# Kernel tuning notes

Hardware: AMD Instinct MI355X
Metric: run time of the kernel (lower is better)

## Reference

```python
import jax, jax.numpy as jnp
import numpy as np
import math

D_MODEL = 1024
NUM_HEADS = 16
HEAD_DIM = D_MODEL // NUM_HEADS
CLAMP = 1e9


def setup_inputs() -> dict:
    key = jax.random.key(0)
    k1, k2, k3, k4, k5 = jax.random.split(key, 5)
    B, S = 2, 2048
    x = jax.random.normal(k1, (B, S, D_MODEL), dtype=jnp.float32)
    # torch Linear params, stored as [in, out] (y = x @ W + b)
    s1 = 1.0 / math.sqrt(D_MODEL)
    W_qkv = jax.random.uniform(k2, (D_MODEL, 3 * D_MODEL), jnp.float32, -s1, s1)
    b_qkv = jax.random.uniform(k3, (3 * D_MODEL,), jnp.float32, -s1, s1)
    W_out = jax.random.uniform(k4, (D_MODEL, D_MODEL), jnp.float32, -s1, s1)
    b_out = jax.random.uniform(k5, (D_MODEL,), jnp.float32, -s1, s1)
    return {"x": x, "W_qkv": W_qkv, "b_qkv": b_qkv, "W_out": W_out, "b_out": b_out}


def reference(x, W_qkv, b_qkv, W_out, b_out):
    B, S, D = x.shape
    qkv = x @ W_qkv + b_qkv                       # [B, S, 3*D]
    qkv = qkv.reshape(B, S, NUM_HEADS, 3 * HEAD_DIM).transpose(0, 2, 1, 3)  # [B, H, S, 3*hd]
    q, k, v = jnp.split(qkv, 3, axis=-1)          # each [B, H, S, hd]
    scale = 1.0 / math.sqrt(HEAD_DIM)
    scores = jnp.einsum('bhqd,bhkd->bhqk', q, k) * scale  # [B, H, S, S]
    causal = jnp.tril(jnp.ones((S, S), dtype=bool))
    scores = jnp.where(causal, scores, -jnp.inf)
    scores = jnp.clip(scores, -CLAMP, CLAMP)      # -inf -> -1e9, matching torch clamp
    attn = jax.nn.softmax(scores, axis=-1)
    values = jnp.einsum('bhqk,bhkd->bhqd', attn, v)        # [B, H, S, hd]
    values = values.transpose(0, 2, 1, 3).reshape(B, S, D)  # [B, S, D]
    out = values @ W_out + b_out
    # dropout is identity in eval mode
    return out
```

## Files before the change

### kernel.cpp

```cpp
#include <hip/hip_runtime.h>
#include <hip/hip_bf16.h>

#define D_MODEL 1024
#define NUM_HEADS 16
#define HEAD_DIM 64
#define SEQ 2048
#define BATCH 2
#define ROWS (BATCH * SEQ)

typedef unsigned short u16;
typedef __bf16 bf16x8 __attribute__((ext_vector_type(8)));
typedef float f32x4 __attribute__((ext_vector_type(4)));

__device__ inline u16 f2bfu(float f) {
  unsigned u = __float_as_uint(f);
  unsigned r = (u + 0x7fffu + ((u >> 16) & 1u)) >> 16;
  return (u16)r;
}

__device__ inline unsigned cvt_pk_bf16(float a, float b) {
#if __has_builtin(__builtin_amdgcn_cvt_pk_bf16_f32)
  auto r = __builtin_amdgcn_cvt_pk_bf16_f32(a, b);
  unsigned u;
  __builtin_memcpy(&u, &r, 4);
  return u;
#else
  return (unsigned)f2bfu(a) | ((unsigned)f2bfu(b) << 16);
#endif
}

__device__ inline f32x4 mfma16(bf16x8 a, bf16x8 b, f32x4 c) {
  return __builtin_amdgcn_mfma_f32_16x16x32_bf16(a, b, c, 0, 0, 0);
}

__device__ inline bf16x8 load_frag(const u16* p) {
  union { uint4 v; bf16x8 f; } u;
  u.v = *(const uint4*)p;
  return u.f;
}

__device__ inline void gload_lds16(const u16* g, u16* l) {
  __builtin_amdgcn_global_load_lds((const __attribute__((address_space(1))) void*)g,
                                   (__attribute__((address_space(3))) void*)l, 16, 0, 0);
}


__global__ __launch_bounds__(256) void prep_kernel(const float* __restrict__ x,
                                                   u16* __restrict__ xb,
                                                   const float* __restrict__ Wq,
                                                   u16* __restrict__ WqT,
                                                   const float* __restrict__ Wo,
                                                   u16* __restrict__ WoT) {
  __shared__ float t[32][33];
  const int bid = blockIdx.x;
  if (bid < 4096) {
    int i = bid * 256 + threadIdx.x;
    float4 v = ((const float4*)x)[i];
    uint2 o;
    o.x = cvt_pk_bf16(v.x, v.y);
    o.y = cvt_pk_bf16(v.z, v.w);
    ((uint2*)xb)[i] = o;
    return;
  }
  const float* W;
  u16* Wt;
  int N, tIdx;
  if (bid < 4096 + 3072) { W = Wq; Wt = WqT; N = 3072; tIdx = bid - 4096; }
  else                   { W = Wo; Wt = WoT; N = 1024; tIdx = bid - 7168; }
  const int k0 = (tIdx & 31) * 32, n0 = (tIdx >> 5) * 32;
  const int c = threadIdx.x & 31, r8 = threadIdx.x >> 5;
#pragma unroll
  for (int i = 0; i < 4; i++) {
    int r = r8 + i * 8;
    t[r][c] = W[(size_t)(k0 + r) * N + n0 + c];
  }
  __syncthreads();
#pragma unroll
  for (int i = 0; i < 4; i++) {
    int r = r8 + i * 8;
    Wt[(size_t)(n0 + r) * 1024 + k0 + c] = f2bfu(t[c][r]);
  }
}


__global__ __launch_bounds__(256, 3) void gemm_qkv(const u16* __restrict__ A,
                                                   const u16* __restrict__ Bt,
                                                   const float* __restrict__ bias,
                                                   u16* __restrict__ Qb, u16* __restrict__ Kb,
                                                   u16* __restrict__ Vt) {
  __shared__ u16 lA[3][128 * 32], lB[3][128 * 32];
  const int tid = threadIdx.x;
  const int wave = tid >> 6, lane = tid & 63, ln = lane & 15, quad = lane >> 4;
  const int lin = blockIdx.y * 24 + blockIdx.x;
  const int reg = lin & 7, idx = lin >> 3;
  const int mr = idx / 12, nr = idx - mr * 12;
  const int m0 = ((reg >> 1) * 8 + mr) * 128;
  const int n0 = (((reg & 1) * 12) + nr) * 128;
  const int wm = (wave & 1) * 64, wn = (wave >> 1) * 64;
  f32x4 acc[4][4] = {};

  auto issue = [&](u16* dA, u16* dB, int k0) {
#pragma unroll
    for (int i = 0; i < 2; ++i) {
      int rb = wave * 2 + i;
      gload_lds16(A + (size_t)(m0 + rb * 16 + ln) * 1024 + k0 + quad * 8, dA + rb * 512);
      gload_lds16(Bt + (size_t)(n0 + rb * 16 + ln) * 1024 + k0 + quad * 8, dB + rb * 512);
    }
  };
  auto compute = [&](const u16* sA, const u16* sB) {
    bf16x8 a[4], b[4];
#pragma unroll
    for (int i = 0; i < 4; ++i) {
      a[i] = load_frag(sA + (wm / 16 + i) * 512 + quad * 128 + ln * 8);
      b[i] = load_frag(sB + (wn / 16 + i) * 512 + quad * 128 + ln * 8);
    }
#pragma unroll
    for (int mt = 0; mt < 4; ++mt)
#pragma unroll
      for (int nt = 0; nt < 4; ++nt) acc[mt][nt] = mfma16(a[mt], b[nt], acc[mt][nt]);
  };

  issue(lA[0], lB[0], 0);
  issue(lA[1], lB[1], 32);
  asm volatile("s_waitcnt vmcnt(4)" ::: "memory");
  asm volatile("s_barrier" ::: "memory");

  for (int tt = 0; tt < 10; ++tt) {
    const int t = tt * 3;
    issue(lA[2], lB[2], (t + 2) * 32);
    compute(lA[0], lB[0]);
    asm volatile("s_waitcnt vmcnt(4)" ::: "memory");
    asm volatile("s_barrier" ::: "memory");
    issue(lA[0], lB[0], (t + 3) * 32);
    compute(lA[1], lB[1]);
    asm volatile("s_waitcnt vmcnt(4)" ::: "memory");
    asm volatile("s_barrier" ::: "memory");
    issue(lA[1], lB[1], (t + 4) * 32);
    compute(lA[2], lB[2]);
    asm volatile("s_waitcnt vmcnt(4)" ::: "memory");
    asm volatile("s_barrier" ::: "memory");
  }
  compute(lA[0], lB[0]);
  asm volatile("s_waitcnt vmcnt(0)" ::: "memory");
  asm volatile("s_barrier" ::: "memory");
  compute(lA[1], lB[1]);

#pragma unroll
  for (int mt = 0; mt < 4; ++mt) {
    int row = m0 + wm + mt * 16 + quad * 4;
    int bb = row >> 11, s0 = row & 2047;
#pragma unroll
    for (int nt = 0; nt < 4; ++nt) {
      int col = n0 + wn + nt * 16 + ln;
      float bv = bias[col];
      int h = col / 192, rem = col - h * 192, t3 = rem >> 6, d = rem & 63;
      int bh = bb * NUM_HEADS + h;
      if (t3 == 2) {
        uint2 pk;
        pk.x = cvt_pk_bf16(acc[mt][nt][0] + bv, acc[mt][nt][1] + bv);
        pk.y = cvt_pk_bf16(acc[mt][nt][2] + bv, acc[mt][nt][3] + bv);
        *(uint2*)(Vt + ((size_t)bh * 64 + d) * SEQ + s0) = pk;
      } else {
        u16* dst = (t3 == 0) ? Qb : Kb;
#pragma unroll
        for (int r = 0; r < 4; ++r)
          dst[((size_t)bh * SEQ + s0 + r) * 64 + d] = f2bfu(acc[mt][nt][r] + bv);
      }
    }
  }
}


__global__ __launch_bounds__(512) void attn_kernel(const u16* __restrict__ Qb,
                                                   const u16* __restrict__ Kb,
                                                   const u16* __restrict__ Vt,
                                                   u16* __restrict__ Ob) {
  __shared__ u16 lK[2 * 2 * 64 * 64];
  __shared__ u16 lV[2 * 64 * 64];
  __shared__ u16 lP[8][1152];
  const int tid = threadIdx.x;
  const int wave = tid >> 6, lane = tid & 63;
  const int ln = lane & 15, quad = lane >> 4;
  const int lin = blockIdx.y * 16 + blockIdx.x;
  const int xreg = lin & 7, xidx = lin >> 3;
  const int j = xidx & 15;
  const int bh = xreg * 4 + (xidx >> 4);
  const int lo = j, hi = 31 - j;
  const int myt = (wave < 4) ? lo : hi;
  const int q0w = myt * 64 + (wave & 3) * 16;
  const int sD = myt >> 1;
  const int nsup = (hi + 2) >> 1;
  const u16* Qg = Qb + (size_t)bh * SEQ * 64;
  const u16* Kg = Kb + (size_t)bh * SEQ * 64;
  const u16* Vg = Vt + (size_t)bh * 64 * SEQ;
  u16* lPw = lP[wave];

  bf16x8 qf[2];
#pragma unroll
  for (int ks = 0; ks < 2; ++ks)
    qf[ks] = load_frag(Qg + (size_t)(q0w + ln) * 64 + ks * 32 + quad * 8);

  const u16* sp[4];
  u16* dp[4];
#pragma unroll
  for (int i = 0; i < 4; ++i) {
    if (wave < 4) {
      int c = wave * 4 + i, half = c >> 3, cc = c & 7, rb = cc >> 1, kgh = cc & 1;
      sp[i] = Kg + (size_t)(half * 64 + rb * 16 + ln) * 64 + (kgh * 4 + quad) * 8;
      dp[i] = lK + half * 4096 + rb * 1024 + kgh * 512;
    } else {
      int c2 = wave * 4 - 16 + i, half = c2 >> 3, cc = c2 & 7, rb = cc >> 1, kgh = cc & 1;
      sp[i] = Vg + (size_t)(rb * 16 + ln) * SEQ + half * 64 + (kgh * 4 + quad) * 8;
      dp[i] = lV + half * 4096 + rb * 1024 + kgh * 512;
    }
  }
  if (wave < 4) {
#pragma unroll
    for (int i = 0; i < 4; ++i) gload_lds16(sp[i], dp[i]);
  }

  f32x4 o[4] = {};
  float m_r = -1e30f;
  float l_r = 0.f;
  const float SC = 0.18033688011112042f;
  const int qq = q0w + ln;

  for (int s = 0; s < nsup; ++s) {
    __syncthreads();
    if (wave >= 4) {
#pragma unroll
      for (int i = 0; i < 4; ++i) gload_lds16(sp[i] + (size_t)s * 128, dp[i]);
    }

    if (s <= sD) {
      const u16* lKs = lK + (s & 1) * 8192;
      f32x4 sc[2][4] = {};
      __builtin_amdgcn_s_setprio(1);
#pragma unroll
      for (int h = 0; h < 2; ++h)
#pragma unroll
        for (int mt = 0; mt < 4; ++mt)
#pragma unroll
          for (int ks = 0; ks < 2; ++ks) {
            bf16x8 kf = load_frag(lKs + h * 4096 + mt * 1024 + (ks * 4 + quad) * 128 + ln * 8);
            sc[h][mt] = mfma16(kf, qf[ks], sc[h][mt]);
          }
      __builtin_amdgcn_s_setprio(0);
      if (s == sD) {
#pragma unroll
        for (int h = 0; h < 2; ++h)
#pragma unroll
          for (int mt = 0; mt < 4; ++mt) {
            int key0 = (2 * s + h) * 64 + mt * 16 + quad * 4;
#pragma unroll
            for (int r = 0; r < 4; ++r)
              if (key0 + r > qq) sc[h][mt][r] = -1e30f;
          }
      }
      float mloc = sc[0][0][0];
#pragma unroll
      for (int h = 0; h < 2; ++h)
#pragma unroll
        for (int mt = 0; mt < 4; ++mt)
#pragma unroll
          for (int r = 0; r < 4; ++r) mloc = fmaxf(mloc, sc[h][mt][r]);
      mloc = fmaxf(mloc, __shfl_xor(mloc, 16));
      mloc = fmaxf(mloc, __shfl_xor(mloc, 32));
      if (!__all(mloc - m_r <= 44.0f)) {
        float mnew = fmaxf(m_r, mloc);
        float alpha = __builtin_amdgcn_exp2f((m_r - mnew) * SC);
        l_r *= alpha;
#pragma unroll
        for (int dt = 0; dt < 4; ++dt) o[dt] *= alpha;
        m_r = mnew;
      }
      float nmsc = -m_r * SC;
      float sum = 0.f;
#pragma unroll
      for (int h = 0; h < 2; ++h)
#pragma unroll
        for (int mt = 0; mt < 4; ++mt)
#pragma unroll
          for (int r = 0; r < 4; ++r) {
            float p = __builtin_amdgcn_exp2f(__builtin_fmaf(sc[h][mt][r], SC, nmsc));
            sc[h][mt][r] = p;
            sum += p;
          }
      sum += __shfl_xor(sum, 16);
      sum += __shfl_xor(sum, 32);
      l_r += sum;

      __syncthreads();
      if (wave < 4 && s + 1 < nsup) {
#pragma unroll
        for (int i = 0; i < 4; ++i)
          gload_lds16(sp[i] + (size_t)(s + 1) * (128 * 64), dp[i] + ((s + 1) & 1) * 8192);
      }

#pragma unroll
      for (int h = 0; h < 2; ++h) {
#pragma unroll
        for (int mt = 0; mt < 4; ++mt) {
          uint2 pk;
          pk.x = cvt_pk_bf16(sc[h][mt][0], sc[h][mt][1]);
          pk.y = cvt_pk_bf16(sc[h][mt][2], sc[h][mt][3]);
          int addr = ln * 64 + (((mt * 2 + (quad >> 1)) ^ (ln & 7)) * 8) + (quad & 1) * 4;
          *(uint2*)(lPw + addr) = pk;
        }
        bf16x8 pf[2];
#pragma unroll
        for (int ks = 0; ks < 2; ++ks)
          pf[ks] = load_frag(lPw + ln * 64 + (((ks * 4 + quad) ^ (ln & 7)) * 8));
        __builtin_amdgcn_s_setprio(1);
#pragma unroll
        for (int dt = 0; dt < 4; ++dt)
#pragma unroll
          for (int ks = 0; ks < 2; ++ks) {
            bf16x8 av = load_frag(lV + h * 4096 + dt * 1024 + (ks * 4 + quad) * 128 + ln * 8);
            o[dt] = mfma16(av, pf[ks], o[dt]);
          }
        __builtin_amdgcn_s_setprio(0);
      }
    } else {
      __syncthreads();
      if (wave < 4 && s + 1 < nsup) {
#pragma unroll
        for (int i = 0; i < 4; ++i)
          gload_lds16(sp[i] + (size_t)(s + 1) * (128 * 64), dp[i] + ((s + 1) & 1) * 8192);
      }
    }
  }

  float inv = 1.f / l_r;
#pragma unroll
  for (int dt = 0; dt < 4; ++dt) {
    uint2 pk;
    pk.x = cvt_pk_bf16(o[dt][0] * inv, o[dt][1] * inv);
    pk.y = cvt_pk_bf16(o[dt][2] * inv, o[dt][3] * inv);
    *(uint2*)(lPw + ln * 72 + dt * 16 + quad * 4) = pk;
  }
  const int b = bh >> 4, h2 = bh & 15;
#pragma unroll
  for (int i = 0; i < 2; ++i) {
    int c = lane + i * 64;
    int qq2 = c >> 3, dg = c & 7;
    uint4 val = *(const uint4*)(lPw + qq2 * 72 + dg * 8);
    *(uint4*)(Ob + ((size_t)b * SEQ + q0w + qq2) * 1024 + h2 * 64 + dg * 8) = val;
  }
}


__global__ __launch_bounds__(256, 2) void gemm_out(const u16* __restrict__ A,
                                                   const u16* __restrict__ Bt,
                                                   const float* __restrict__ bias,
                                                   float* __restrict__ out) {
  __shared__ u16 lA[3][128 * 64], lB[3][64 * 64];
  const int tid = threadIdx.x;
  const int wave = tid >> 6, lane = tid & 63, ln = lane & 15, quad = lane >> 4;
  const int lin = blockIdx.y * 16 + blockIdx.x;
  const int reg = lin & 7, idx = lin >> 3;
  const int mr = idx >> 3, nr = idx & 7;
  const int m0 = ((reg >> 1) * 8 + mr) * 128;
  const int n0 = (((reg & 1) * 8) + nr) * 64;
  f32x4 acc[2][4] = {};

  auto issue = [&](u16* dA, u16* dB, int k0) {
#pragma unroll
    for (int i = 0; i < 6; ++i) {
      int c = wave * 6 + i;
      if (c < 16) {
        int kh = c & 1, rb = c >> 1;
        gload_lds16(A + (size_t)(m0 + rb * 16 + ln) * 1024 + k0 + kh * 32 + quad * 8,
                    dA + kh * 4096 + rb * 512);
      } else {
        int c2 = c - 16, kh = c2 & 1, rbn = c2 >> 1;
        gload_lds16(Bt + (size_t)(n0 + rbn * 16 + ln) * 1024 + k0 + kh * 32 + quad * 8,
                    dB + kh * 2048 + rbn * 512);
      }
    }
  };
  auto compute = [&](const u16* sA, const u16* sB) {
    bf16x8 a[2][2], b[4][2];
#pragma unroll
    for (int ks = 0; ks < 2; ++ks) {
#pragma unroll
      for (int i = 0; i < 2; ++i)
        a[i][ks] = load_frag(sA + ks * 4096 + (wave * 2 + i) * 512 + quad * 128 + ln * 8);
#pragma unroll
      for (int i = 0; i < 4; ++i)
        b[i][ks] = load_frag(sB + ks * 2048 + i * 512 + quad * 128 + ln * 8);
    }
#pragma unroll
    for (int ks = 0; ks < 2; ++ks)
#pragma unroll
      for (int mt = 0; mt < 2; ++mt)
#pragma unroll
        for (int nt = 0; nt < 4; ++nt)
          acc[mt][nt] = mfma16(a[mt][ks], b[nt][ks], acc[mt][nt]);
  };

  issue(lA[0], lB[0], 0);
  issue(lA[1], lB[1], 64);
  asm volatile("s_waitcnt vmcnt(6)" ::: "memory");
  asm volatile("s_barrier" ::: "memory");

  for (int tt = 0; tt < 4; ++tt) {
    const int t = tt * 3;
    issue(lA[2], lB[2], (t + 2) * 64);
    compute(lA[0], lB[0]);
    asm volatile("s_waitcnt vmcnt(6)" ::: "memory");
    asm volatile("s_barrier" ::: "memory");
    issue(lA[0], lB[0], (t + 3) * 64);
    compute(lA[1], lB[1]);
    asm volatile("s_waitcnt vmcnt(6)" ::: "memory");
    asm volatile("s_barrier" ::: "memory");
    issue(lA[1], lB[1], (t + 4) * 64);
    compute(lA[2], lB[2]);
    asm volatile("s_waitcnt vmcnt(6)" ::: "memory");
    asm volatile("s_barrier" ::: "memory");
  }
  issue(lA[2], lB[2], 14 * 64);
  compute(lA[0], lB[0]);
  asm volatile("s_waitcnt vmcnt(6)" ::: "memory");
  asm volatile("s_barrier" ::: "memory");
  issue(lA[0], lB[0], 15 * 64);
  compute(lA[1], lB[1]);
  asm volatile("s_waitcnt vmcnt(6)" ::: "memory");
  asm volatile("s_barrier" ::: "memory");
  compute(lA[2], lB[2]);
  asm volatile("s_waitcnt vmcnt(0)" ::: "memory");
  asm volatile("s_barrier" ::: "memory");
  compute(lA[0], lB[0]);

#pragma unroll
  for (int mt = 0; mt < 2; ++mt) {
    int row = m0 + wave * 32 + mt * 16 + quad * 4;
#pragma unroll
    for (int nt = 0; nt < 4; ++nt) {
      int col = n0 + nt * 16 + ln;
      float bv = bias[col];
#pragma unroll
      for (int r = 0; r < 4; ++r)
        out[(size_t)(row + r) * 1024 + col] = acc[mt][nt][r] + bv;
    }
  }
}


extern "C" void kernel_launch(void* const* d_in, const int* in_sizes, int n_in,
                              void* d_out, int out_size, void* d_ws, size_t ws_size,
                              hipStream_t stream) {
  const float* x = (const float*)d_in[0];
  const float* W_qkv = (const float*)d_in[1];
  const float* b_qkv = (const float*)d_in[2];
  const float* W_out = (const float*)d_in[3];
  const float* b_out = (const float*)d_in[4];
  float* out = (float*)d_out;

  char* ws = (char*)d_ws;
  const size_t SZ_XB = (size_t)ROWS * D_MODEL * 2;
  const size_t SZ_WQKVT = (size_t)3 * D_MODEL * D_MODEL * 2;
  const size_t SZ_WOUTT = (size_t)D_MODEL * D_MODEL * 2;
  const size_t SZ_HEADS = (size_t)BATCH * NUM_HEADS * SEQ * HEAD_DIM * 2;
  u16* xb = (u16*)(ws);
  u16* WqkvT = (u16*)(ws + SZ_XB);
  u16* WoutT = (u16*)(ws + SZ_XB + SZ_WQKVT);
  u16* Qb = (u16*)(ws + SZ_XB + SZ_WQKVT + SZ_WOUTT);
  u16* Kb = (u16*)(ws + SZ_XB + SZ_WQKVT + SZ_WOUTT + SZ_HEADS);
  u16* Vt = (u16*)(ws + SZ_XB + SZ_WQKVT + SZ_WOUTT + 2 * SZ_HEADS);
  u16* Ob = (u16*)(ws + SZ_XB + SZ_WQKVT + SZ_WOUTT + 3 * SZ_HEADS);

  prep_kernel<<<dim3(8192), dim3(256), 0, stream>>>(x, xb, W_qkv, WqkvT, W_out, WoutT);
  gemm_qkv<<<dim3(3 * D_MODEL / 128, ROWS / 128), dim3(256), 0, stream>>>(xb, WqkvT, b_qkv,
                                                                          Qb, Kb, Vt);
  attn_kernel<<<dim3(SEQ / 128, BATCH * NUM_HEADS), dim3(512), 0, stream>>>(Qb, Kb, Vt, Ob);
  gemm_out<<<dim3(D_MODEL / 64, ROWS / 128), dim3(256), 0, stream>>>(Ob, WoutT, b_out, out);
}
```

Baseline: 200.7 us.

## Skip masked diagonal half-tile, tree-reduce softmax, double-buffer out-proj GEMM for occupancy

In the attention kernel, the second 64-key half of the diagonal super-tile is skipped when it is fully masked for a given wave: both the QK MFMAs and the PV MFMAs for that half are elided. The softmax max and sum reductions become tree-shaped to shorten dependency chains. The output-projection GEMM switches from triple to double buffering in LDS with launch bounds raised to 3 blocks per CU, trading prefetch depth for occupancy and adding an extra barrier per stage.

```diff
diff --git a/kernel.cpp b/kernel.cpp
--- a/kernel.cpp
+++ b/kernel.cpp
@@ -233,11 +233,13 @@
     }
 
     if (s <= sD) {
+      const bool skip1 = (s == sD) && !(myt & 1);
       const u16* lKs = lK + (s & 1) * 8192;
       f32x4 sc[2][4] = {};
       __builtin_amdgcn_s_setprio(1);
 #pragma unroll
-      for (int h = 0; h < 2; ++h)
+      for (int h = 0; h < 2; ++h) {
+        if (h == 1 && skip1) continue;
 #pragma unroll
         for (int mt = 0; mt < 4; ++mt)
 #pragma unroll
@@ -245,6 +247,7 @@
             bf16x8 kf = load_frag(lKs + h * 4096 + mt * 1024 + (ks * 4 + quad) * 128 + ln * 8);
             sc[h][mt] = mfma16(kf, qf[ks], sc[h][mt]);
           }
+      }
       __builtin_amdgcn_s_setprio(0);
       if (s == sD) {
 #pragma unroll
@@ -257,13 +260,15 @@
               if (key0 + r > qq) sc[h][mt][r] = -1e30f;
           }
       }
-      float mloc = sc[0][0][0];
+      float m8[8];
 #pragma unroll
       for (int h = 0; h < 2; ++h)
 #pragma unroll
         for (int mt = 0; mt < 4; ++mt)
-#pragma unroll
-          for (int r = 0; r < 4; ++r) mloc = fmaxf(mloc, sc[h][mt][r]);
+          m8[h * 4 + mt] = fmaxf(fmaxf(sc[h][mt][0], sc[h][mt][1]),
+                                 fmaxf(sc[h][mt][2], sc[h][mt][3]));
+      float mloc = fmaxf(fmaxf(fmaxf(m8[0], m8[1]), fmaxf(m8[2], m8[3])),
+                         fmaxf(fmaxf(m8[4], m8[5]), fmaxf(m8[6], m8[7])));
       mloc = fmaxf(mloc, __shfl_xor(mloc, 16));
       mloc = fmaxf(mloc, __shfl_xor(mloc, 32));
       if (!__all(mloc - m_r <= 44.0f)) {
@@ -275,7 +280,7 @@
         m_r = mnew;
       }
       float nmsc = -m_r * SC;
-      float sum = 0.f;
+      float s4[4] = {0.f, 0.f, 0.f, 0.f};
 #pragma unroll
       for (int h = 0; h < 2; ++h)
 #pragma unroll
@@ -284,8 +289,9 @@
           for (int r = 0; r < 4; ++r) {
             float p = __builtin_amdgcn_exp2f(__builtin_fmaf(sc[h][mt][r], SC, nmsc));
             sc[h][mt][r] = p;
-            sum += p;
+            s4[r] += p;
           }
+      float sum = (s4[0] + s4[1]) + (s4[2] + s4[3]);
       sum += __shfl_xor(sum, 16);
       sum += __shfl_xor(sum, 32);
       l_r += sum;
@@ -299,6 +305,7 @@
 
 #pragma unroll
       for (int h = 0; h < 2; ++h) {
+        if (h == 1 && skip1) continue;
 #pragma unroll
         for (int mt = 0; mt < 4; ++mt) {
           uint2 pk;
@@ -350,11 +357,11 @@
 }
 
 
-__global__ __launch_bounds__(256, 2) void gemm_out(const u16* __restrict__ A,
+__global__ __launch_bounds__(256, 3) void gemm_out(const u16* __restrict__ A,
                                                    const u16* __restrict__ Bt,
                                                    const float* __restrict__ bias,
                                                    float* __restrict__ out) {
-  __shared__ u16 lA[3][128 * 64], lB[3][64 * 64];
+  __shared__ u16 lA[2][128 * 64], lB[2][64 * 64];
   const int tid = threadIdx.x;
   const int wave = tid >> 6, lane = tid & 63, ln = lane & 15, quad = lane >> 4;
   const int lin = blockIdx.y * 16 + blockIdx.x;
@@ -400,37 +407,26 @@
   };
 
   issue(lA[0], lB[0], 0);
-  issue(lA[1], lB[1], 64);
+  for (int p = 0; p < 7; ++p) {
+    asm volatile("s_barrier" ::: "memory");
+    issue(lA[1], lB[1], (2 * p + 1) * 64);
+    asm volatile("s_waitcnt vmcnt(6)" ::: "memory");
+    asm volatile("s_barrier" ::: "memory");
+    compute(lA[0], lB[0]);
+    asm volatile("s_barrier" ::: "memory");
+    issue(lA[0], lB[0], (2 * p + 2) * 64);
+    asm volatile("s_waitcnt vmcnt(6)" ::: "memory");
+    asm volatile("s_barrier" ::: "memory");
+    compute(lA[1], lB[1]);
+  }
+  asm volatile("s_barrier" ::: "memory");
+  issue(lA[1], lB[1], 15 * 64);
   asm volatile("s_waitcnt vmcnt(6)" ::: "memory");
   asm volatile("s_barrier" ::: "memory");
-
-  for (int tt = 0; tt < 4; ++tt) {
-    const int t = tt * 3;
-    issue(lA[2], lB[2], (t + 2) * 64);
-    compute(lA[0], lB[0]);
-    asm volatile("s_waitcnt vmcnt(6)" ::: "memory");
-    asm volatile("s_barrier" ::: "memory");
-    issue(lA[0], lB[0], (t + 3) * 64);
-    compute(lA[1], lB[1]);
-    asm volatile("s_waitcnt vmcnt(6)" ::: "memory");
-    asm volatile("s_barrier" ::: "memory");
-    issue(lA[1], lB[1], (t + 4) * 64);
-    compute(lA[2], lB[2]);
-    asm volatile("s_waitcnt vmcnt(6)" ::: "memory");
-    asm volatile("s_barrier" ::: "memory");
-  }
-  issue(lA[2], lB[2], 14 * 64);
   compute(lA[0], lB[0]);
-  asm volatile("s_waitcnt vmcnt(6)" ::: "memory");
-  asm volatile("s_barrier" ::: "memory");
-  issue(lA[0], lB[0], 15 * 64);
-  compute(lA[1], lB[1]);
-  asm volatile("s_waitcnt vmcnt(6)" ::: "memory");
-  asm volatile("s_barrier" ::: "memory");
-  compute(lA[2], lB[2]);
   asm volatile("s_waitcnt vmcnt(0)" ::: "memory");
   asm volatile("s_barrier" ::: "memory");
-  compute(lA[0], lB[0]);
+  compute(lA[1], lB[1]);
 
 #pragma unroll
   for (int mt = 0; mt < 2; ++mt) {
```

Result: no change. 202.2 us (+0.7%).
